# Optimization experiments

Measured on AMD Instinct MI355X. Metric: run time of the kernel, lower is better.

## Reference

```python
import jax, jax.numpy as jnp
import numpy as np

N = 50000   # nodes
E = 800000  # edges (avg degree 16)
H = 128     # hidden


def setup_inputs() -> dict:
    key = jax.random.key(0)
    ks = jax.random.split(key, 10)
    s = 1.0 / np.sqrt(H)
    x = jax.random.normal(ks[0], (N, H), jnp.float32)
    src = jax.random.randint(ks[1], (E,), 0, N)
    dst = jax.random.randint(ks[2], (E,), 0, N)
    edge_index = jnp.stack([src, dst]).astype(jnp.int64)
    def lin(k, shape, scale):
        return (jax.random.normal(k, shape, jnp.float32) * scale)
    return {
        "x": x,
        "edge_index": edge_index,
        "W1": lin(ks[3], (H, H), s), "b1": jnp.zeros((H,), jnp.float32),
        "W2": lin(ks[4], (H, H), s), "b2": jnp.zeros((H,), jnp.float32),
        "W3": lin(ks[5], (H, H), s), "b3": jnp.zeros((H,), jnp.float32),
        "gw1": lin(ks[6], (H, 1), s), "gb1": jnp.zeros((1,), jnp.float32),
        "gw2": lin(ks[7], (H, 1), s), "gb2": jnp.zeros((1,), jnp.float32),
        "gw3": lin(ks[8], (H, 1), s), "gb3": jnp.zeros((1,), jnp.float32),
    }


def _gcn_layer(x, W, b, src, dst):
    # PyG GCNConv with self-loops and symmetric normalization.
    h = x @ W                                                   # [N, H]
    deg = jax.ops.segment_sum(jnp.ones((E,), h.dtype), dst, num_segments=N) + 1.0
    dinv = jax.lax.rsqrt(deg)                                   # deg^-0.5, [N]
    norm = dinv[src] * dinv[dst]                                # [E]
    agg = jax.ops.segment_sum(norm[:, None] * h[src], dst, num_segments=N)
    agg = agg + (dinv * dinv)[:, None] * h                      # self-loop term
    return agg + b


def _att_pool(x, gw, gb):
    # GlobalAttention with batch == zeros: single-graph softmax pooling.
    gate = jax.nn.sigmoid(x @ gw + gb)          # [N, 1]
    a = jax.nn.softmax(gate, axis=0)            # [N, 1]
    return jnp.sum(a * x, axis=0, keepdims=True)  # [1, H]


def reference(x, edge_index, W1, b1, W2, b2, W3, b3,
              gw1, gb1, gw2, gb2, gw3, gb3):
    src, dst = edge_index[0], edge_index[1]
    x1 = jax.nn.relu(_gcn_layer(x, W1, b1, src, dst))
    r1 = _att_pool(x1, gw1, gb1)
    x2 = jax.nn.relu(_gcn_layer(x1, W2, b2, src, dst))
    r2 = _att_pool(x2, gw2, gb2)
    x3 = jax.nn.relu(_gcn_layer(x2, W3, b3, src, dst))
    r3 = _att_pool(x3, gw3, gb3)
    return jnp.concatenate([r1, r2, r3], axis=1)  # [1, 3H]
```

## Files before the change

kernel.cpp:

```cpp
#include <hip/hip_runtime.h>
#include <hip/hip_bf16.h>

#define NN 50000
#define EE 800000
#define HH 128
#define BCAP 64

typedef __attribute__((ext_vector_type(8))) short bf16x8;
typedef __attribute__((ext_vector_type(8))) unsigned short u16x8;
typedef __attribute__((ext_vector_type(4))) float f32x4;

#define OFF_HBF    0
#define OFF_ABF    (NN * HH / 2)
#define OFF_DEG    (NN * HH)
#define OFF_DINV   (OFF_DEG + NN)
#define OFF_BUCKET (OFF_DINV + NN)
#define OFF_S      (OFF_BUCKET + NN * BCAP)
#define OFF_WHP    (OFF_S + 4)
#define OFF_WLP    (OFF_WHP + 24576)

__device__ inline unsigned short f2bf(float f) {
    unsigned u = __float_as_uint(f);
    u += 0x7fffu + ((u >> 16) & 1u);
    return (unsigned short)(u >> 16);
}
__device__ inline float bf2f(unsigned short h) {
    unsigned u = ((unsigned)h) << 16;
    return __uint_as_float(u);
}

__global__ void k_fill(const int* __restrict__ ei, int* __restrict__ deg,
                       int* __restrict__ bucket) {
    int e = blockIdx.x * 256 + threadIdx.x;
    if (e >= EE) return;
    int s = ei[e];
    int d = ei[EE + e];
    int c = atomicAdd(&deg[d], 1);
    if (c < BCAP) bucket[d * BCAP + c] = s;
}

__global__ void k_dinv(const int* __restrict__ deg, float* __restrict__ d) {
    int n = blockIdx.x * 256 + threadIdx.x;
    if (n < NN) d[n] = rsqrtf((float)deg[n] + 1.0f);
}

__global__ void k_wprep(const float* __restrict__ Wa, const float* __restrict__ Wb,
                        const float* __restrict__ Wc,
                        short* __restrict__ Whp, short* __restrict__ Wlp) {
    int g = blockIdx.x * 256 + threadIdx.x;
    if (g >= 3 * 2048) return;
    int layer = g >> 11;
    int r = g & 2047;
    int ct = r >> 8, ks = (r >> 6) & 3, lane = r & 63;
    const float* W = (layer == 0) ? Wa : (layer == 1) ? Wb : Wc;
    int kbase = ks * 32 + ((lane >> 4) << 3);
    int n = ct * 16 + (lane & 15);
    #pragma unroll
    for (int j = 0; j < 8; ++j) {
        float w = W[(kbase + j) * HH + n];
        unsigned short hi = f2bf(w);
        unsigned short lo = f2bf(w - bf2f(hi));
        Whp[(size_t)layer * 16384 + r * 8 + j] = (short)hi;
        Wlp[(size_t)layer * 16384 + r * 8 + j] = (short)lo;
    }
}

__global__ void k_cvt(const float* __restrict__ X, short* __restrict__ Xbf) {
    int i = blockIdx.x * 256 + threadIdx.x;
    float4 v = ((const float4*)X)[i];
    ushort4 o;
    o.x = f2bf(v.x); o.y = f2bf(v.y); o.z = f2bf(v.z); o.w = f2bf(v.w);
    ((ushort4*)Xbf)[i] = o;
}

__global__ __launch_bounds__(256) void k_gemm(
        const short* __restrict__ Xbf, const short* __restrict__ Whp,
        const short* __restrict__ Wlp, const float* __restrict__ dinv,
        short* __restrict__ Hout) {
    int t = threadIdx.x;
    int lane = t & 63;
    int wv = t >> 6;
    int row0 = blockIdx.x * 64 + wv * 16;
    int arow = row0 + (lane & 15);
    int koff = (lane >> 4) << 3;

    bf16x8 a[4];
    #pragma unroll
    for (int ks = 0; ks < 4; ++ks) {
        if (arow < NN)
            a[ks] = *(const bf16x8*)(Xbf + (size_t)arow * HH + ks * 32 + koff);
        else
            a[ks] = (bf16x8)(short)0;
    }

    const bf16x8* Bh = (const bf16x8*)Whp;
    const bf16x8* Bl = (const bf16x8*)Wlp;
    int crow0 = row0 + ((lane >> 4) << 2);
    int ccol = lane & 15;

    float dsc[4];
    #pragma unroll
    for (int r = 0; r < 4; ++r) {
        int cr = crow0 + r;
        dsc[r] = (cr < NN) ? dinv[cr] : 0.f;
    }

    #pragma unroll
    for (int ct = 0; ct < 8; ++ct) {
        f32x4 acc = {0.f, 0.f, 0.f, 0.f};
        #pragma unroll
        for (int ks = 0; ks < 4; ++ks)
            acc = __builtin_amdgcn_mfma_f32_16x16x32_bf16(a[ks], Bh[(ct * 4 + ks) * 64 + lane], acc, 0, 0, 0);
        #pragma unroll
        for (int ks = 0; ks < 4; ++ks)
            acc = __builtin_amdgcn_mfma_f32_16x16x32_bf16(a[ks], Bl[(ct * 4 + ks) * 64 + lane], acc, 0, 0, 0);
        #pragma unroll
        for (int r = 0; r < 4; ++r) {
            int cr = crow0 + r;
            if (cr < NN)
                Hout[(size_t)cr * HH + ct * 16 + ccol] = (short)f2bf(dsc[r] * acc[r]);
        }
    }
}

__global__ __launch_bounds__(256) void k_gather(
        const short* __restrict__ Hs, const int* __restrict__ deg,
        const int* __restrict__ bucket, const float* __restrict__ dinv,
        const float* __restrict__ bias, short* __restrict__ Abf) {
    int t = threadIdx.x;
    int node = blockIdx.x * 16 + (t >> 4);
    int c8 = (t & 15) << 3;
    int cnt = deg[node];
    if (cnt > BCAP) cnt = BCAP;
    const int* bp = bucket + (size_t)node * BCAP;

    float acc[8];
    {
        u16x8 hv = *(const u16x8*)(Hs + (size_t)node * HH + c8);
        #pragma unroll
        for (int j = 0; j < 8; ++j) acc[j] = bf2f(hv[j]);
    }

    int e = 0;
    for (; e + 4 <= cnt; e += 4) {
        int s0 = bp[e], s1 = bp[e + 1], s2 = bp[e + 2], s3 = bp[e + 3];
        u16x8 v0 = *(const u16x8*)(Hs + (size_t)s0 * HH + c8);
        u16x8 v1 = *(const u16x8*)(Hs + (size_t)s1 * HH + c8);
        u16x8 v2 = *(const u16x8*)(Hs + (size_t)s2 * HH + c8);
        u16x8 v3 = *(const u16x8*)(Hs + (size_t)s3 * HH + c8);
        #pragma unroll
        for (int j = 0; j < 8; ++j)
            acc[j] += (bf2f(v0[j]) + bf2f(v1[j])) + (bf2f(v2[j]) + bf2f(v3[j]));
    }
    for (; e < cnt; ++e) {
        int s = bp[e];
        u16x8 v = *(const u16x8*)(Hs + (size_t)s * HH + c8);
        #pragma unroll
        for (int j = 0; j < 8; ++j) acc[j] += bf2f(v[j]);
    }

    float di = dinv[node];
    const float4 bv0 = *(const float4*)(bias + c8);
    const float4 bv1 = *(const float4*)(bias + c8 + 4);
    float bb[8] = {bv0.x, bv0.y, bv0.z, bv0.w, bv1.x, bv1.y, bv1.z, bv1.w};
    u16x8 o;
    #pragma unroll
    for (int j = 0; j < 8; ++j)
        o[j] = f2bf(fmaxf(di * acc[j] + bb[j], 0.f));
    *(u16x8*)(Abf + (size_t)node * HH + c8) = o;
}

__global__ __launch_bounds__(256) void k_pool(
        const short* __restrict__ X, const float* __restrict__ gw,
        const float* __restrict__ gbp, float* __restrict__ outp,
        float* __restrict__ Sp) {
    __shared__ float red[HH];
    int t = threadIdx.x;
    int lane = t & 63;
    int wid = blockIdx.x * 4 + (t >> 6);
    int nw = gridDim.x * 4;
    float gb = gbp[0];
    float gw0 = gw[2 * lane], gw1 = gw[2 * lane + 1];
    float acc0 = 0.f, acc1 = 0.f, sE = 0.f;
    for (int n = wid; n < NN; n += nw) {
        ushort2 xv = *(const ushort2*)(X + (size_t)n * HH + 2 * lane);
        float x0 = bf2f(xv.x), x1 = bf2f(xv.y);
        float p = x0 * gw0 + x1 * gw1;
        #pragma unroll
        for (int m = 32; m >= 1; m >>= 1) p += __shfl_xor(p, m, 64);
        float g = 1.f / (1.f + expf(-(p + gb)));
        float e = expf(g);
        acc0 += e * x0;
        acc1 += e * x1;
        if (lane == 0) sE += e;
    }
    if (t < HH) red[t] = 0.f;
    __syncthreads();
    atomicAdd(&red[2 * lane], acc0);
    atomicAdd(&red[2 * lane + 1], acc1);
    __syncthreads();
    if (lane == 0) atomicAdd(Sp, sE);
    if (t < HH) atomicAdd(&outp[t], red[t]);
}

__global__ void k_scale(float* __restrict__ outp, const float* __restrict__ Sp) {
    int i = blockIdx.x * 256 + threadIdx.x;
    if (i < 3 * HH) outp[i] /= Sp[i >> 7];
}

extern "C" void kernel_launch(void* const* d_in, const int* in_sizes, int n_in,
                              void* d_out, int out_size, void* d_ws, size_t ws_size,
                              hipStream_t stream) {
    const float* x  = (const float*)d_in[0];
    const int* ei   = (const int*)d_in[1];
    const float* W1 = (const float*)d_in[2]; const float* b1 = (const float*)d_in[3];
    const float* W2 = (const float*)d_in[4]; const float* b2 = (const float*)d_in[5];
    const float* W3 = (const float*)d_in[6]; const float* b3 = (const float*)d_in[7];
    const float* gw1 = (const float*)d_in[8];  const float* gb1 = (const float*)d_in[9];
    const float* gw2 = (const float*)d_in[10]; const float* gb2 = (const float*)d_in[11];
    const float* gw3 = (const float*)d_in[12]; const float* gb3 = (const float*)d_in[13];
    float* out = (float*)d_out;
    float* ws  = (float*)d_ws;

    short* Hbf    = (short*)(ws + OFF_HBF);
    short* Abf    = (short*)(ws + OFF_ABF);
    int*   deg    = (int*)(ws + OFF_DEG);
    float* dinv   = ws + OFF_DINV;
    int*   bucket = (int*)(ws + OFF_BUCKET);
    float* S      = ws + OFF_S;
    short* Whp    = (short*)(ws + OFF_WHP);
    short* Wlp    = (short*)(ws + OFF_WLP);

    hipMemsetAsync(deg, 0, NN * sizeof(int), stream);
    hipMemsetAsync(S, 0, 16, stream);
    hipMemsetAsync(out, 0, 3 * HH * sizeof(float), stream);

    const int EG = (EE + 255) / 256;
    const int NG = (NN + 255) / 256;
    k_fill<<<EG, 256, 0, stream>>>(ei, deg, bucket);
    k_dinv<<<NG, 256, 0, stream>>>(deg, dinv);
    k_wprep<<<24, 256, 0, stream>>>(W1, W2, W3, Whp, Wlp);
    k_cvt<<<(NN * HH / 4 + 255) / 256, 256, 0, stream>>>(x, Abf);

    const int GEMM_GRID = (NN + 63) / 64;
    const int GATH_GRID = (NN + 15) / 16;

    k_gemm<<<GEMM_GRID, 256, 0, stream>>>(Abf, Whp, Wlp, dinv, Hbf);
    k_gather<<<GATH_GRID, 256, 0, stream>>>(Hbf, deg, bucket, dinv, b1, Abf);
    k_pool<<<512, 256, 0, stream>>>(Abf, gw1, gb1, out, S);
    k_gemm<<<GEMM_GRID, 256, 0, stream>>>(Abf, Whp + 16384, Wlp + 16384, dinv, Hbf);
    k_gather<<<GATH_GRID, 256, 0, stream>>>(Hbf, deg, bucket, dinv, b2, Abf);
    k_pool<<<512, 256, 0, stream>>>(Abf, gw2, gb2, out + HH, S + 1);
    k_gemm<<<GEMM_GRID, 256, 0, stream>>>(Abf, Whp + 32768, Wlp + 32768, dinv, Hbf);
    k_gather<<<GATH_GRID, 256, 0, stream>>>(Hbf, deg, bucket, dinv, b3, Abf);
    k_pool<<<512, 256, 0, stream>>>(Abf, gw3, gb3, out + 2 * HH, S + 2);

    k_scale<<<2, 256, 0, stream>>>(out, S);
}
```

Measured before the change: 412.9 us.

## Shard bucket fill by destination, stage GEMM output in LDS, fold dinv into consumers

```diff
diff --git a/kernel.cpp b/kernel.cpp
--- a/kernel.cpp
+++ b/kernel.cpp
@@ -4,7 +4,11 @@
 #define NN 50000
 #define EE 800000
 #define HH 128
+#define HHP 136
 #define BCAP 64
+#define NSHARD 8
+#define SHW 6250
+#define FCH 391
 
 typedef __attribute__((ext_vector_type(8))) short bf16x8;
 typedef __attribute__((ext_vector_type(8))) unsigned short u16x8;
@@ -13,8 +17,7 @@
 #define OFF_HBF    0
 #define OFF_ABF    (NN * HH / 2)
 #define OFF_DEG    (NN * HH)
-#define OFF_DINV   (OFF_DEG + NN)
-#define OFF_BUCKET (OFF_DINV + NN)
+#define OFF_BUCKET (OFF_DEG + NN)
 #define OFF_S      (OFF_BUCKET + NN * BCAP)
 #define OFF_WHP    (OFF_S + 4)
 #define OFF_WLP    (OFF_WHP + 24576)
@@ -29,19 +32,28 @@
     return __uint_as_float(u);
 }
 
+__global__ void k_zero(int* __restrict__ deg, float* __restrict__ S,
+                       float* __restrict__ outp) {
+    int i = blockIdx.x * 256 + threadIdx.x;
+    if (i < NN) deg[i] = 0;
+    if (i < 4) S[i] = 0.f;
+    if (i < 3 * HH) outp[i] = 0.f;
+}
+
 __global__ void k_fill(const int* __restrict__ ei, int* __restrict__ deg,
                        int* __restrict__ bucket) {
-    int e = blockIdx.x * 256 + threadIdx.x;
-    if (e >= EE) return;
-    int s = ei[e];
-    int d = ei[EE + e];
-    int c = atomicAdd(&deg[d], 1);
-    if (c < BCAP) bucket[d * BCAP + c] = s;
-}
-
-__global__ void k_dinv(const int* __restrict__ deg, float* __restrict__ d) {
-    int n = blockIdx.x * 256 + threadIdx.x;
-    if (n < NN) d[n] = rsqrtf((float)deg[n] + 1.0f);
+    int b = blockIdx.x;
+    int shard = b & (NSHARD - 1);
+    int chunk = b >> 3;
+    int lo = shard * SHW, hi = lo + SHW;
+    for (int e = chunk * 256 + threadIdx.x; e < EE; e += FCH * 256) {
+        int d = ei[EE + e];
+        if (d >= lo && d < hi) {
+            int s = ei[e];
+            int c = atomicAdd(&deg[d], 1);
+            if (c < BCAP) bucket[d * BCAP + c] = s;
+        }
+    }
 }
 
 __global__ void k_wprep(const float* __restrict__ Wa, const float* __restrict__ Wb,
@@ -75,8 +87,9 @@
 
 __global__ __launch_bounds__(256) void k_gemm(
         const short* __restrict__ Xbf, const short* __restrict__ Whp,
-        const short* __restrict__ Wlp, const float* __restrict__ dinv,
+        const short* __restrict__ Wlp, const int* __restrict__ deg,
         short* __restrict__ Hout) {
+    __shared__ short Ls[4 * 16 * HHP];
     int t = threadIdx.x;
     int lane = t & 63;
     int wv = t >> 6;
@@ -95,16 +108,17 @@
 
     const bf16x8* Bh = (const bf16x8*)Whp;
     const bf16x8* Bl = (const bf16x8*)Wlp;
-    int crow0 = row0 + ((lane >> 4) << 2);
+    int crow0l = (lane >> 4) << 2;
     int ccol = lane & 15;
 
     float dsc[4];
     #pragma unroll
     for (int r = 0; r < 4; ++r) {
-        int cr = crow0 + r;
-        dsc[r] = (cr < NN) ? dinv[cr] : 0.f;
-    }
-
+        int cr = row0 + crow0l + r;
+        dsc[r] = (cr < NN) ? rsqrtf((float)deg[cr] + 1.0f) : 0.f;
+    }
+
+    short* Lw = Ls + wv * (16 * HHP);
     #pragma unroll
     for (int ct = 0; ct < 8; ++ct) {
         f32x4 acc = {0.f, 0.f, 0.f, 0.f};
@@ -115,23 +129,33 @@
         for (int ks = 0; ks < 4; ++ks)
             acc = __builtin_amdgcn_mfma_f32_16x16x32_bf16(a[ks], Bl[(ct * 4 + ks) * 64 + lane], acc, 0, 0, 0);
         #pragma unroll
-        for (int r = 0; r < 4; ++r) {
-            int cr = crow0 + r;
-            if (cr < NN)
-                Hout[(size_t)cr * HH + ct * 16 + ccol] = (short)f2bf(dsc[r] * acc[r]);
-        }
+        for (int r = 0; r < 4; ++r)
+            Lw[(crow0l + r) * HHP + ct * 16 + ccol] = (short)f2bf(dsc[r] * acc[r]);
+    }
+    __syncthreads();
+
+    #pragma unroll
+    for (int it = 0; it < 4; ++it) {
+        int chunk = it * 64 + lane;
+        int row = chunk >> 4;
+        int c8 = (chunk & 15) << 3;
+        int grow = row0 + row;
+        if (grow < NN)
+            *(u16x8*)(Hout + (size_t)grow * HH + c8) =
+                *(const u16x8*)(Lw + row * HHP + c8);
     }
 }
 
 __global__ __launch_bounds__(256) void k_gather(
         const short* __restrict__ Hs, const int* __restrict__ deg,
-        const int* __restrict__ bucket, const float* __restrict__ dinv,
-        const float* __restrict__ bias, short* __restrict__ Abf) {
+        const int* __restrict__ bucket, const float* __restrict__ bias,
+        short* __restrict__ Abf) {
     int t = threadIdx.x;
     int node = blockIdx.x * 16 + (t >> 4);
     int c8 = (t & 15) << 3;
-    int cnt = deg[node];
-    if (cnt > BCAP) cnt = BCAP;
+    int cd = deg[node];
+    float di = rsqrtf((float)cd + 1.0f);
+    int cnt = (cd > BCAP) ? BCAP : cd;
     const int* bp = bucket + (size_t)node * BCAP;
 
     float acc[8];
@@ -159,7 +183,6 @@
         for (int j = 0; j < 8; ++j) acc[j] += bf2f(v[j]);
     }
 
-    float di = dinv[node];
     const float4 bv0 = *(const float4*)(bias + c8);
     const float4 bv1 = *(const float4*)(bias + c8 + 4);
     float bb[8] = {bv0.x, bv0.y, bv0.z, bv0.w, bv1.x, bv1.y, bv1.z, bv1.w};
@@ -225,34 +248,27 @@
     short* Hbf    = (short*)(ws + OFF_HBF);
     short* Abf    = (short*)(ws + OFF_ABF);
     int*   deg    = (int*)(ws + OFF_DEG);
-    float* dinv   = ws + OFF_DINV;
     int*   bucket = (int*)(ws + OFF_BUCKET);
     float* S      = ws + OFF_S;
     short* Whp    = (short*)(ws + OFF_WHP);
     short* Wlp    = (short*)(ws + OFF_WLP);
 
-    hipMemsetAsync(deg, 0, NN * sizeof(int), stream);
-    hipMemsetAsync(S, 0, 16, stream);
-    hipMemsetAsync(out, 0, 3 * HH * sizeof(float), stream);
-
-    const int EG = (EE + 255) / 256;
-    const int NG = (NN + 255) / 256;
-    k_fill<<<EG, 256, 0, stream>>>(ei, deg, bucket);
-    k_dinv<<<NG, 256, 0, stream>>>(deg, dinv);
+    k_zero<<<(NN + 255) / 256, 256, 0, stream>>>(deg, S, out);
+    k_fill<<<NSHARD * FCH, 256, 0, stream>>>(ei, deg, bucket);
     k_wprep<<<24, 256, 0, stream>>>(W1, W2, W3, Whp, Wlp);
     k_cvt<<<(NN * HH / 4 + 255) / 256, 256, 0, stream>>>(x, Abf);
 
     const int GEMM_GRID = (NN + 63) / 64;
-    const int GATH_GRID = (NN + 15) / 16;
-
-    k_gemm<<<GEMM_GRID, 256, 0, stream>>>(Abf, Whp, Wlp, dinv, Hbf);
-    k_gather<<<GATH_GRID, 256, 0, stream>>>(Hbf, deg, bucket, dinv, b1, Abf);
+    const int GATH_GRID = NN / 16;
+
+    k_gemm<<<GEMM_GRID, 256, 0, stream>>>(Abf, Whp, Wlp, deg, Hbf);
+    k_gather<<<GATH_GRID, 256, 0, stream>>>(Hbf, deg, bucket, b1, Abf);
     k_pool<<<512, 256, 0, stream>>>(Abf, gw1, gb1, out, S);
-    k_gemm<<<GEMM_GRID, 256, 0, stream>>>(Abf, Whp + 16384, Wlp + 16384, dinv, Hbf);
-    k_gather<<<GATH_GRID, 256, 0, stream>>>(Hbf, deg, bucket, dinv, b2, Abf);
+    k_gemm<<<GEMM_GRID, 256, 0, stream>>>(Abf, Whp + 16384, Wlp + 16384, deg, Hbf);
+    k_gather<<<GATH_GRID, 256, 0, stream>>>(Hbf, deg, bucket, b2, Abf);
     k_pool<<<512, 256, 0, stream>>>(Abf, gw2, gb2, out + HH, S + 1);
-    k_gemm<<<GEMM_GRID, 256, 0, stream>>>(Abf, Whp + 32768, Wlp + 32768, dinv, Hbf);
-    k_gather<<<GATH_GRID, 256, 0, stream>>>(Hbf, deg, bucket, dinv, b3, Abf);
+    k_gemm<<<GEMM_GRID, 256, 0, stream>>>(Abf, Whp + 32768, Wlp + 32768, deg, Hbf);
+    k_gather<<<GATH_GRID, 256, 0, stream>>>(Hbf, deg, bucket, b3, Abf);
     k_pool<<<512, 256, 0, stream>>>(Abf, gw3, gb3, out + 2 * HH, S + 2);
 
     k_scale<<<2, 256, 0, stream>>>(out, S);
```

After: 394.2 us. 4.5% less time.
